# Performance work log

Measured on AMD Instinct MI355X. Metric: run time of the kernel, lower is better.

The kernel has to match this reference:

```python
import jax, jax.numpy as jnp
import numpy as np
from jax import lax

BS, EN, SEQ = 512, 512, 64
D_ENT, D_IN, D_KEY, D_F, H = 256, 1024, 32, 256, 32


def _layer_norm(x, g, b, eps=1e-5):
    m = x.mean(-1, keepdims=True)
    v = ((x - m) ** 2).mean(-1, keepdims=True)
    return (x - m) * lax.rsqrt(v + eps) * g + b


def setup_inputs() -> dict:
    key = jax.random.key(0)
    ks = jax.random.split(key, 24)
    f32 = jnp.float32

    def w(k, shape, fan_in):
        return (jax.random.normal(k, shape, dtype=f32) / np.sqrt(fan_in)).astype(f32)

    inp = {
        'entity_embedding': jax.random.normal(ks[0], (BS, EN, D_ENT), dtype=f32),
        'autoregressive_embedding': jax.random.normal(ks[1], (BS, D_IN), dtype=f32),
        'entity_num': jax.random.randint(ks[2], (BS,), 0, EN),
        'selected_units': jax.random.randint(ks[3], (BS, SEQ), 0, EN),
        'selected_units_num': jax.random.randint(ks[4], (BS,), 0, SEQ),
        # fc_block params (Linear: y = x @ W + b)
        'key_fc_w': w(ks[5], (D_ENT, D_KEY), D_ENT), 'key_fc_b': jnp.zeros((D_KEY,), f32),
        'q1_w': w(ks[6], (D_IN, D_F), D_IN), 'q1_b': jnp.zeros((D_F,), f32),
        'q2_w': w(ks[7], (D_F, D_KEY), D_F), 'q2_b': jnp.zeros((D_KEY,), f32),
        'e1_w': w(ks[8], (D_KEY, D_F), D_KEY), 'e1_b': jnp.zeros((D_F,), f32),
        'e2_w': w(ks[9], (D_F, D_IN), D_F), 'e2_b': jnp.zeros((D_IN,), f32),
        'end_embedding': jax.random.uniform(ks[10], (D_KEY,), dtype=f32,
                                            minval=-1.0 / np.sqrt(D_KEY), maxval=1.0 / np.sqrt(D_KEY)),
        # LayerNorm-LSTM (single layer), gate order: i, f, g, o
        'w_ih': w(ks[11], (D_KEY, 4 * H), D_KEY),
        'w_hh': w(ks[12], (H, 4 * H), H),
        'ln_ig': 1.0 + 0.1 * jax.random.normal(ks[13], (4 * H,), dtype=f32),
        'ln_ib': 0.1 * jax.random.normal(ks[14], (4 * H,), dtype=f32),
        'ln_hg': 1.0 + 0.1 * jax.random.normal(ks[15], (4 * H,), dtype=f32),
        'ln_hb': 0.1 * jax.random.normal(ks[16], (4 * H,), dtype=f32),
        'ln_cg': 1.0 + 0.1 * jax.random.normal(ks[17], (H,), dtype=f32),
        'ln_cb': 0.1 * jax.random.normal(ks[18], (H,), dtype=f32),
    }
    return inp


def _forward(entity_embedding, autoregressive_embedding, entity_num, selected_units,
             selected_units_num, key_fc_w, key_fc_b, q1_w, q1_b, q2_w, q2_b,
             e1_w, e1_b, e2_w, e2_b, end_embedding,
             w_ih, w_hh, ln_ig, ln_ib, ln_hg, ln_hb, ln_cg, ln_cb):
    bs = entity_embedding.shape[0]
    ar = jnp.arange(bs)
    # _get_key_mask: keys for all entities + zero pad slot, end_embedding at slot entity_num
    key = entity_embedding @ key_fc_w + key_fc_b                      # [bs, EN, Dk]
    key = jnp.concatenate([key, jnp.zeros((bs, 1, key.shape[-1]), key.dtype)], axis=1)  # [bs, EN+1, Dk]
    key = key.at[ar, entity_num].set(end_embedding.astype(key.dtype))
    key_embeddings = key                                              # reduce_type == 'selected_units_num'
    base_mask = jnp.arange(key.shape[1])[None, :] < (entity_num + 1)[:, None]  # sequence_mask(entity_num+1)
    mask0 = base_mask.at[ar, entity_num].set(False)                   # end token masked at step 0
    su_prev = jnp.concatenate([selected_units[:, :1], selected_units[:, :-1]], axis=1)

    def step(carry, xs):
        mask, ae, end_flag, one_hot, h, c = carry
        i, su_i, su_p = xs
        # teacher-forced mask evolution
        m1 = jnp.where(i == 1, mask.at[ar, entity_num].set(True), mask)
        m2 = m1.at[ar, su_p].set(False)
        mask = jnp.where(i > 0, m2, mask)
        # query_fc2(query_fc1(ae)) -> LN-LSTM cell
        x = jnp.maximum(ae @ q1_w + q1_b, 0.0) @ q2_w + q2_b
        gates = _layer_norm(x @ w_ih, ln_ig, ln_ib) + _layer_norm(h @ w_hh, ln_hg, ln_hb)
        ig, fg, cg, og = jnp.split(gates, 4, axis=-1)
        c = _layer_norm(jax.nn.sigmoid(fg) * c + jax.nn.sigmoid(ig) * jnp.tanh(cg), ln_cg, ln_cb)
        h = jax.nn.sigmoid(og) * jnp.tanh(c)
        # one-hot scatter of selected unit (skipped once end token seen)
        end_flag = end_flag | (su_i == entity_num)
        one_hot = one_hot.at[ar, su_i].max((~end_flag).astype(one_hot.dtype))
        # mean-pooled embedding of selected units -> embed_fc -> new ae
        emb = jnp.einsum('bn,bnd->bd', one_hot, key_embeddings)
        cnt = one_hot.sum(-1)
        denom = jnp.where((selected_units_num != 0) & (cnt > 0), cnt, 1.0)
        emb = emb / denom[:, None]
        ae = autoregressive_embedding + (jnp.maximum(emb @ e1_w + e1_b, 0.0) @ e2_w + e2_b)
        return (mask, ae, end_flag, one_hot, h, c), (h, mask)

    carry0 = (mask0, autoregressive_embedding,
              jnp.zeros((bs,), bool), jnp.zeros((bs, key.shape[1]), key.dtype),
              jnp.zeros((bs, w_hh.shape[0]), key.dtype), jnp.zeros((bs, w_hh.shape[0]), key.dtype))
    xs = (jnp.arange(selected_units.shape[1]), selected_units.T, su_prev.T)
    _, (queries, masks) = lax.scan(step, carry0, xs)   # [S,bs,Dk], [S,bs,EN+1]
    logits = jnp.einsum('sbd,bnd->sbn', queries, key)
    logits = jnp.where(masks, logits, jnp.asarray(-1e9, logits.dtype))
    return logits.transpose(1, 0, 2)                   # [bs, S, EN+1]


def reference(entity_embedding, autoregressive_embedding, entity_num, selected_units,
              selected_units_num, key_fc_w, key_fc_b, q1_w, q1_b, q2_w, q2_b,
              e1_w, e1_b, e2_w, e2_b, end_embedding,
              w_ih, w_hh, ln_ig, ln_ib, ln_hg, ln_hb, ln_cg, ln_cb):
    return _forward(entity_embedding, autoregressive_embedding, entity_num, selected_units,
                    selected_units_num, key_fc_w, key_fc_b, q1_w, q1_b, q2_w, q2_b,
                    e1_w, e1_b, e2_w, e2_b, end_embedding,
                    w_ih, w_hh, ln_ig, ln_ib, ln_hg, ln_hb, ln_cg, ln_cb)
```

## Files before the change

### kernel.cpp

```cpp
#include <hip/hip_runtime.h>
#include <cstdint>
#include <cstddef>


typedef short bf16x8 __attribute__((ext_vector_type(8)));
typedef float f32x4  __attribute__((ext_vector_type(4)));

__device__ __forceinline__ unsigned f2bf2(float lo, float hi) {
    unsigned r;
    asm("v_cvt_pk_bf16_f32 %0, %1, %2" : "=v"(r) : "v"(lo), "v"(hi));
    return r;
}
__device__ __forceinline__ ushort f2bf(float f) {
    unsigned r;
    asm("v_cvt_pk_bf16_f32 %0, %1, %1" : "=v"(r) : "v"(f));
    return (ushort)r;
}

__device__ __forceinline__ void gld16(const void* g, void* l) {
    __builtin_amdgcn_global_load_lds(
        (const __attribute__((address_space(1))) void*)g,
        (__attribute__((address_space(3))) void*)l,
        16, 0, 0);
}

template<int BM, int BN, int BK, int WR, int WC,
         bool RELU, bool ADDVEC, bool OUT_BF16, bool A_F32, bool KEYMODE>
__global__ __launch_bounds__(WR * WC * 64)
void mfma_gemm(const void* __restrict__ Av, int lda,
               const ushort* __restrict__ BT,
               const float* __restrict__ bias,
               const float* __restrict__ addvec, int ldadd,
               void* __restrict__ outv, int ldo,
               int K, int out_row_offset)
{
    constexpr int NT  = WR * WC * 64;
    constexpr int WM  = BM / WR, WN = BN / WC;
    constexpr int TMt = WM / 16, TNt = WN / 16;
    constexpr int KC  = BK / 8;
    constexpr int CHA = BM * KC, CHB = BN * KC;
    __shared__ __align__(16) ushort As[BM * BK];
    __shared__ __align__(16) ushort Bs[BN * BK];

    const int tid  = threadIdx.x;
    const int lane = tid & 63;
    const int w    = tid >> 6;
    const int wr   = w / WC, wc = w % WC;
    const int row0 = blockIdx.x * BM;
    const int n0   = blockIdx.y * BN;

    f32x4 acc[TMt][TNt];
#pragma unroll
    for (int i = 0; i < TMt; i++)
#pragma unroll
        for (int j = 0; j < TNt; j++)
#pragma unroll
            for (int r = 0; r < 4; r++) acc[i][j][r] = 0.f;

    const ushort* Ab = (const ushort*)Av;
    const float*  Af = (const float*)Av;

    for (int k0 = 0; k0 < K; k0 += BK) {
        if (A_F32) {
#pragma unroll
            for (int id = tid; id < CHA; id += NT) {
                int r = id / KC, kc = id % KC;
                const float* src = Af + (size_t)(row0 + r) * lda + k0 + kc * 8;
                float4 v0 = *(const float4*)(src);
                float4 v1 = *(const float4*)(src + 4);
                uint4 p;
                p.x = f2bf2(v0.x, v0.y);
                p.y = f2bf2(v0.z, v0.w);
                p.z = f2bf2(v1.x, v1.y);
                p.w = f2bf2(v1.z, v1.w);
                *(uint4*)(&As[id * 8]) = p;
            }
        } else {
#pragma unroll
            for (int id = tid; id < CHA; id += NT) {
                int r = id / KC, kc = id % KC;
                gld16(Ab + (size_t)(row0 + r) * lda + k0 + kc * 8, &As[id * 8]);
            }
        }
#pragma unroll
        for (int id = tid; id < CHB; id += NT) {
            int r = id / KC, kc = id % KC;
            gld16(BT + (size_t)(n0 + r) * K + k0 + kc * 8, &Bs[id * 8]);
        }
        __syncthreads();

        bf16x8 afr[TMt], bfr[TNt];
        const int krd = (lane >> 4) * 8;
        const int mrd = lane & 15;
#pragma unroll
        for (int tm = 0; tm < TMt; tm++)
            afr[tm] = *(bf16x8*)(&As[(wr * WM + tm * 16 + mrd) * BK + krd]);
#pragma unroll
        for (int tn = 0; tn < TNt; tn++)
            bfr[tn] = *(bf16x8*)(&Bs[(wc * WN + tn * 16 + mrd) * BK + krd]);
#pragma unroll
        for (int tm = 0; tm < TMt; tm++)
#pragma unroll
            for (int tn = 0; tn < TNt; tn++)
                acc[tm][tn] = __builtin_amdgcn_mfma_f32_16x16x32_bf16(
                    afr[tm], bfr[tn], acc[tm][tn], 0, 0, 0);
        __syncthreads();
    }

    float*  outf = (float*)outv;
    ushort* outh = (ushort*)outv;
    const int cn = lane & 15;
    const int rb = (lane >> 4) * 4;
#pragma unroll
    for (int tm = 0; tm < TMt; tm++) {
#pragma unroll
        for (int r = 0; r < 4; r++) {
            int grow = row0 + wr * WM + tm * 16 + rb + r;
            int b_   = grow & 511;
#pragma unroll
            for (int tn = 0; tn < TNt; tn++) {
                int gcol = n0 + wc * WN + tn * 16 + cn;
                float v = acc[tm][tn][r] + bias[gcol];
                if (RELU)   v = fmaxf(v, 0.f);
                if (ADDVEC) v += addvec[(size_t)b_ * ldadd + gcol];
                size_t oidx;
                if (KEYMODE) oidx = ((size_t)(grow >> 9) * 513 + b_) * 32 + gcol;
                else         oidx = (size_t)(grow + out_row_offset) * ldo + gcol;
                if (OUT_BF16) outh[oidx] = f2bf(v);
                else          outf[oidx] = v;
            }
        }
    }
}

__global__ __launch_bounds__(256) void misc_prep(
    const float* __restrict__ kw,  const float* __restrict__ e1w,
    const float* __restrict__ e2w, const float* __restrict__ q1w,
    const float* __restrict__ q2w,
    ushort* __restrict__ kwt,  ushort* __restrict__ e1wt,
    ushort* __restrict__ e2wt, ushort* __restrict__ q1wt,
    ushort* __restrict__ q2wt,
    const float* __restrict__ ar, ushort* __restrict__ AEb)
{
    int bx = blockIdx.x;
    if (bx < 512) {
        int i = (bx * 256 + threadIdx.x) * 4;
        float4 v = *(const float4*)(ar + i);
        uint2 o;
        o.x = f2bf2(v.x, v.y);
        o.y = f2bf2(v.z, v.w);
        *(uint2*)(AEb + i) = o;
        return;
    }
    bx -= 512;
    const float* W; ushort* WT; int K, N, t0;
    if      (bx < 8)   { W = kw;  WT = kwt;  K = 256;  N = 32;   t0 = bx; }
    else if (bx < 16)  { W = e1w; WT = e1wt; K = 32;   N = 256;  t0 = bx - 8; }
    else if (bx < 272) { W = e2w; WT = e2wt; K = 256;  N = 1024; t0 = bx - 16; }
    else if (bx < 528) { W = q1w; WT = q1wt; K = 1024; N = 256;  t0 = bx - 272; }
    else               { W = q2w; WT = q2wt; K = 256;  N = 32;   t0 = bx - 528; }
    int nn = N >> 5;
    int kt = (t0 / nn) * 32, nt = (t0 % nn) * 32;
    __shared__ float t[32][33];
    int x = threadIdx.x & 31, y = threadIdx.x >> 5;
    for (int i = y; i < 32; i += 8) t[i][x] = W[(size_t)(kt + i) * N + nt + x];
    __syncthreads();
    for (int i = y; i < 32; i += 8) WT[(size_t)(nt + i) * K + kt + x] = f2bf(t[x][i]);
}

__global__ __launch_bounds__(64) void prep_kernel(
    const int* __restrict__ en_g, const int* __restrict__ su_g,
    const int* __restrict__ sun_g, float* __restrict__ key,
    const float* __restrict__ eemb,
    int* __restrict__ fs_g, ushort* __restrict__ EMB)
{
    int b = blockIdx.x;
    int tid = threadIdx.x;
    __shared__ int fs_l[513];
    __shared__ int su_l[64];
    __shared__ float krows[64 * 32];
    for (int i = tid; i < 513; i += 64) fs_l[i] = 64;
    su_l[tid] = su_g[b * 64 + tid];
    int en = en_g[b];
    if (tid < 32) key[((size_t)b * 513 + 512) * 32 + tid] = 0.f;
    else          key[((size_t)b * 513 + en) * 32 + (tid - 32)] = eemb[tid - 32];
    __syncthreads();
    atomicMin(&fs_l[su_l[tid]], tid);
    unsigned long long ball = __ballot(su_l[tid] == en);
    int T = ball ? (__ffsll(ball) - 1) : 64;
    __syncthreads();
    {
        int d = tid & 31;
#pragma unroll 4
        for (int i = 0; i < 32; i++) {
            int r = 2 * i + (tid >> 5);
            krows[r * 32 + d] = key[((size_t)b * 513 + su_l[r]) * 32 + d];
        }
    }
    for (int i = tid; i < 513; i += 64) fs_g[(size_t)b * 513 + i] = fs_l[i];
    __syncthreads();

    int sun = sun_g[b];
    float a = 0.f;
    int cnt = 0;
    for (int i = 0; i < 64; i++) {
        bool nw = (i < T) && (fs_l[su_l[i]] == i);
        if (nw) {
            cnt++;
            if (tid < 32) a += krows[i * 32 + tid];
        }
        float denom = (sun != 0 && cnt > 0) ? (float)cnt : 1.0f;
        if (tid < 32) EMB[((size_t)i * 512 + b) * 32 + tid] = f2bf(a / denom);
    }
}

__device__ inline float sigm(float x) { return 1.0f / (1.0f + expf(-x)); }

__global__ __launch_bounds__(128) void lstm_kernel(
    const float* __restrict__ X, const float* __restrict__ wih_g,
    const float* __restrict__ whh_g,
    const float* __restrict__ lnig, const float* __restrict__ lnib,
    const float* __restrict__ lnhg, const float* __restrict__ lnhb,
    const float* __restrict__ lncg, const float* __restrict__ lncb,
    float* __restrict__ Q)
{
    const int wv = threadIdx.x >> 6;
    const int lane = threadIdx.x & 63;
    const int b = blockIdx.x * 2 + wv;
    __shared__ float xs[2][64 * 32];

    {
        int d = lane & 31;
#pragma unroll 8
        for (int i = 0; i < 32; i++) {
            int s = 2 * i + (lane >> 5);
            xs[wv][s * 32 + d] = X[((size_t)s * 512 + b) * 32 + d];
        }
    }
    float w0[32], w1[32], u0[32], u1[32];
#pragma unroll
    for (int k = 0; k < 32; k++) {
        w0[k] = wih_g[k * 128 + lane];
        w1[k] = wih_g[k * 128 + lane + 64];
        u0[k] = whh_g[k * 128 + lane];
        u1[k] = whh_g[k * 128 + lane + 64];
    }
    const float gi0 = lnig[lane], gi1 = lnig[lane + 64];
    const float bi0 = lnib[lane], bi1 = lnib[lane + 64];
    const float gh0 = lnhg[lane], gh1 = lnhg[lane + 64];
    const float bh0 = lnhb[lane], bh1 = lnhb[lane + 64];
    const int j = lane & 31;
    const float gc = lncg[j], bc = lncb[j];
    float h = 0.f, c = 0.f;
    __syncthreads();

    const float* xrow = &xs[wv][0];
    for (int s = 0; s < 64; s++) {
        float ax0 = 0.f, ax1 = 0.f, ah0 = 0.f, ah1 = 0.f;
#pragma unroll
        for (int k = 0; k < 32; k++) {
            float xk = xrow[s * 32 + k];
            float hk = __shfl(h, k);
            ax0 += xk * w0[k]; ax1 += xk * w1[k];
            ah0 += hk * u0[k]; ah1 += hk * u1[k];
        }
        float r0 = ax0 + ax1, r1 = ax0 * ax0 + ax1 * ax1;
        float r2 = ah0 + ah1, r3 = ah0 * ah0 + ah1 * ah1;
#pragma unroll
        for (int m = 1; m <= 32; m <<= 1) {
            r0 += __shfl_xor(r0, m); r1 += __shfl_xor(r1, m);
            r2 += __shfl_xor(r2, m); r3 += __shfl_xor(r3, m);
        }
        float mx = r0 * (1.f / 128.f), vx = r1 * (1.f / 128.f) - mx * mx;
        float mh = r2 * (1.f / 128.f), vh = r3 * (1.f / 128.f) - mh * mh;
        float sx = rsqrtf(vx + 1e-5f), sh = rsqrtf(vh + 1e-5f);
        float g0 = (ax0 - mx) * sx * gi0 + bi0 + (ah0 - mh) * sh * gh0 + bh0;
        float g1 = (ax1 - mx) * sx * gi1 + bi1 + (ah1 - mh) * sh * gh1 + bh1;
        float igv = __shfl(g0, j),      fgv = __shfl(g0, j + 32);
        float cgv = __shfl(g1, j),      ogv = __shfl(g1, j + 32);
        float cc = sigm(fgv) * c + sigm(igv) * tanhf(cgv);
        float s0 = cc, s1 = cc * cc;
#pragma unroll
        for (int m = 1; m <= 32; m <<= 1) {
            s0 += __shfl_xor(s0, m); s1 += __shfl_xor(s1, m);
        }
        float mc = s0 * (1.f / 64.f), vc = s1 * (1.f / 64.f) - mc * mc;
        c = (cc - mc) * rsqrtf(vc + 1e-5f) * gc + bc;
        h = sigm(ogv) * tanhf(c);
        if (lane < 32) Q[((size_t)b * 64 + s) * 32 + lane] = h;
    }
}

__global__ __launch_bounds__(128) void logits_kernel(
    const float* __restrict__ key, const float* __restrict__ Q,
    const int* __restrict__ fs_g, const int* __restrict__ en_g,
    float* __restrict__ out)
{
    int b = blockIdx.x;
    int n0 = blockIdx.y * 128;
    int tid = threadIdx.x;
    __shared__ float Qs[64 * 32];
    __shared__ float Ks[128 * 33];
    for (int i = tid * 4; i < 2048; i += 512)
        *(float4*)(&Qs[i]) = *(const float4*)(Q + (size_t)b * 2048 + i);
    for (int i = tid; i < 4096; i += 128) {
        int r = i >> 5, d = i & 31;
        int n = n0 + r;
        Ks[r * 33 + d] = (n < 513) ? key[((size_t)b * 513 + n) * 32 + d] : 0.f;
    }
    __syncthreads();
    int n = n0 + tid;
    if (n < 513) {
        int en = en_g[b];
        int f = fs_g[(size_t)b * 513 + n];
        float kreg[32];
#pragma unroll
        for (int d = 0; d < 32; d++) kreg[d] = Ks[tid * 33 + d];
        for (int s = 0; s < 64; s++) {
            float a = 0.f;
#pragma unroll
            for (int d = 0; d < 32; d++) a += Qs[s * 32 + d] * kreg[d];
            bool m = (s == 0) ? (n < en) : ((n <= en) && (f >= s));
            out[((size_t)b * 64 + s) * 513 + n] = m ? a : -1e9f;
        }
    }
}

extern "C" void kernel_launch(void* const* d_in, const int* in_sizes, int n_in,
                              void* d_out, int out_size, void* d_ws, size_t ws_size,
                              hipStream_t stream)
{
    const float* ee   = (const float*)d_in[0];
    const float* ar   = (const float*)d_in[1];
    const int*   en   = (const int*)d_in[2];
    const int*   su   = (const int*)d_in[3];
    const int*   sun  = (const int*)d_in[4];
    const float* kw   = (const float*)d_in[5];
    const float* kb   = (const float*)d_in[6];
    const float* q1w  = (const float*)d_in[7];
    const float* q1b  = (const float*)d_in[8];
    const float* q2w  = (const float*)d_in[9];
    const float* q2b  = (const float*)d_in[10];
    const float* e1w  = (const float*)d_in[11];
    const float* e1b  = (const float*)d_in[12];
    const float* e2w  = (const float*)d_in[13];
    const float* e2b  = (const float*)d_in[14];
    const float* eemb = (const float*)d_in[15];
    const float* wih  = (const float*)d_in[16];
    const float* whh  = (const float*)d_in[17];
    const float* lnig = (const float*)d_in[18];
    const float* lnib = (const float*)d_in[19];
    const float* lnhg = (const float*)d_in[20];
    const float* lnhb = (const float*)d_in[21];
    const float* lncg = (const float*)d_in[22];
    const float* lncb = (const float*)d_in[23];
    float* outp = (float*)d_out;

    char* p = (char*)d_ws;
    float*  key  = (float*)p;  p += (size_t)512 * 513 * 32 * 4;
    ushort* AEb  = (ushort*)p; p += (size_t)32768 * 1024 * 2;
    ushort* Z1b  = (ushort*)p; p += (size_t)32768 * 256 * 2;
    ushort* EMBb = (ushort*)p; p += (size_t)32768 * 32 * 2;
    float*  X    = (float*)p;  p += (size_t)32768 * 32 * 4;
    float*  Q    = (float*)p;  p += (size_t)32768 * 32 * 4;
    int*    fs   = (int*)p;    p += (size_t)512 * 513 * 4;
    ushort* kwt  = (ushort*)p; p += (size_t)32 * 256 * 2;
    ushort* e1wt = (ushort*)p; p += (size_t)256 * 32 * 2;
    ushort* e2wt = (ushort*)p; p += (size_t)1024 * 256 * 2;
    ushort* q1wt = (ushort*)p; p += (size_t)256 * 1024 * 2;
    ushort* q2wt = (ushort*)p; p += (size_t)32 * 256 * 2;

    misc_prep<<<1048, 256, 0, stream>>>(kw, e1w, e2w, q1w, q2w,
                                        kwt, e1wt, e2wt, q1wt, q2wt, ar, AEb);

    mfma_gemm<128, 32, 32, 4, 1, false, false, false, true, true>
        <<<dim3(2048, 1), 256, 0, stream>>>(ee, 256, kwt, kb, nullptr, 0, key, 32, 256, 0);
    prep_kernel<<<512, 64, 0, stream>>>(en, su, sun, key, eemb, fs, EMBb);

    mfma_gemm<128, 128, 32, 2, 2, true, false, true, false, false>
        <<<dim3(252, 2), 256, 0, stream>>>(EMBb, 32, e1wt, e1b, nullptr, 0, Z1b, 256, 32, 0);
    mfma_gemm<128, 128, 32, 2, 2, false, true, true, false, false>
        <<<dim3(252, 8), 256, 0, stream>>>(Z1b, 256, e2wt, e2b, ar, 1024, AEb, 1024, 256, 512);
    mfma_gemm<128, 128, 32, 2, 2, true, false, true, false, false>
        <<<dim3(256, 2), 256, 0, stream>>>(AEb, 1024, q1wt, q1b, nullptr, 0, Z1b, 256, 1024, 0);
    mfma_gemm<128, 32, 32, 4, 1, false, false, false, false, false>
        <<<dim3(256, 1), 256, 0, stream>>>(Z1b, 256, q2wt, q2b, nullptr, 0, X, 32, 256, 0);

    lstm_kernel<<<256, 128, 0, stream>>>(X, wih, whh, lnig, lnib, lnhg, lnhb, lncg, lncb, Q);

    logits_kernel<<<dim3(512, 5), 128, 0, stream>>>(key, Q, fs, en, outp);
}
```

Baseline: 699.0 us.

## Swizzle GEMM LDS tiles, raise BK, add A-panel-resident e2 GEMM kernel

Adds an XOR swizzle to the LDS layout of the generic MFMA GEMM to cut bank conflicts on fragment reads, and generalises the inner loop so BK can be raised to 64 for several GEMMs. It adds a dedicated kernel for the e2 projection that keeps a 64x256 A panel in LDS and loops over all eight N tiles, so A is loaded once instead of once per N block. It also vectorises Q reads from LDS in the logits kernel. The price is more LDS per block, which may lower occupancy, plus a serial N loop inside the new kernel.

```diff
diff --git a/kernel.cpp b/kernel.cpp
--- a/kernel.cpp
+++ b/kernel.cpp
@@ -38,6 +38,7 @@
     constexpr int WM  = BM / WR, WN = BN / WC;
     constexpr int TMt = WM / 16, TNt = WN / 16;
     constexpr int KC  = BK / 8;
+    constexpr int SWZ = KC - 1;
     constexpr int CHA = BM * KC, CHB = BN * KC;
     __shared__ __align__(16) ushort As[BM * BK];
     __shared__ __align__(16) ushort Bs[BN * BK];
@@ -65,7 +66,8 @@
 #pragma unroll
             for (int id = tid; id < CHA; id += NT) {
                 int r = id / KC, kc = id % KC;
-                const float* src = Af + (size_t)(row0 + r) * lda + k0 + kc * 8;
+                int kcs = kc ^ (r & SWZ);
+                const float* src = Af + (size_t)(row0 + r) * lda + k0 + kcs * 8;
                 float4 v0 = *(const float4*)(src);
                 float4 v1 = *(const float4*)(src + 4);
                 uint4 p;
@@ -79,31 +81,42 @@
 #pragma unroll
             for (int id = tid; id < CHA; id += NT) {
                 int r = id / KC, kc = id % KC;
-                gld16(Ab + (size_t)(row0 + r) * lda + k0 + kc * 8, &As[id * 8]);
+                int kcs = kc ^ (r & SWZ);
+                gld16(Ab + (size_t)(row0 + r) * lda + k0 + kcs * 8, &As[id * 8]);
             }
         }
 #pragma unroll
         for (int id = tid; id < CHB; id += NT) {
             int r = id / KC, kc = id % KC;
-            gld16(BT + (size_t)(n0 + r) * K + k0 + kc * 8, &Bs[id * 8]);
+            int kcs = kc ^ (r & SWZ);
+            gld16(BT + (size_t)(n0 + r) * K + k0 + kcs * 8, &Bs[id * 8]);
         }
         __syncthreads();
 
-        bf16x8 afr[TMt], bfr[TNt];
-        const int krd = (lane >> 4) * 8;
-        const int mrd = lane & 15;
-#pragma unroll
-        for (int tm = 0; tm < TMt; tm++)
-            afr[tm] = *(bf16x8*)(&As[(wr * WM + tm * 16 + mrd) * BK + krd]);
-#pragma unroll
-        for (int tn = 0; tn < TNt; tn++)
-            bfr[tn] = *(bf16x8*)(&Bs[(wc * WN + tn * 16 + mrd) * BK + krd]);
-#pragma unroll
-        for (int tm = 0; tm < TMt; tm++)
-#pragma unroll
-            for (int tn = 0; tn < TNt; tn++)
-                acc[tm][tn] = __builtin_amdgcn_mfma_f32_16x16x32_bf16(
-                    afr[tm], bfr[tn], acc[tm][tn], 0, 0, 0);
+        const int m16 = lane & 15;
+        const int hi  = lane >> 4;
+#pragma unroll
+        for (int kk = 0; kk < BK / 32; kk++) {
+            bf16x8 afr[TMt], bfr[TNt];
+#pragma unroll
+            for (int tm = 0; tm < TMt; tm++) {
+                int row = wr * WM + tm * 16 + m16;
+                int cc  = kk * 4 + hi;
+                afr[tm] = *(bf16x8*)(&As[row * BK + ((cc ^ (row & SWZ)) << 3)]);
+            }
+#pragma unroll
+            for (int tn = 0; tn < TNt; tn++) {
+                int row = wc * WN + tn * 16 + m16;
+                int cc  = kk * 4 + hi;
+                bfr[tn] = *(bf16x8*)(&Bs[row * BK + ((cc ^ (row & SWZ)) << 3)]);
+            }
+#pragma unroll
+            for (int tm = 0; tm < TMt; tm++)
+#pragma unroll
+                for (int tn = 0; tn < TNt; tn++)
+                    acc[tm][tn] = __builtin_amdgcn_mfma_f32_16x16x32_bf16(
+                        afr[tm], bfr[tn], acc[tm][tn], 0, 0, 0);
+        }
         __syncthreads();
     }
 
@@ -128,6 +141,94 @@
                 else         oidx = (size_t)(grow + out_row_offset) * ldo + gcol;
                 if (OUT_BF16) outh[oidx] = f2bf(v);
                 else          outf[oidx] = v;
+            }
+        }
+    }
+}
+
+__global__ __launch_bounds__(256) void gemm_g4_panel(
+    const ushort* __restrict__ Z1,
+    const ushort* __restrict__ BT,
+    const float* __restrict__ bias,
+    const float* __restrict__ ar,
+    ushort* __restrict__ out)
+{
+    __shared__ __align__(16) ushort Ap[64 * 256];
+    __shared__ __align__(16) ushort Bs[128 * 64];
+
+    const int tid  = threadIdx.x;
+    const int lane = tid & 63;
+    const int w    = tid >> 6;
+    const int wr   = w >> 1, wc = w & 1;
+    const int row0 = blockIdx.x * 64;
+
+#pragma unroll
+    for (int id = tid; id < 2048; id += 256) {
+        int r = id >> 5, c = id & 31;
+        int cs = c ^ (r & 7);
+        gld16(Z1 + (size_t)(row0 + r) * 256 + cs * 8, &Ap[id * 8]);
+    }
+    __syncthreads();
+
+    const int m16 = lane & 15;
+    const int hi  = lane >> 4;
+    const int cn  = lane & 15;
+    const int rb  = (lane >> 4) * 4;
+
+    for (int by = 0; by < 8; by++) {
+        f32x4 acc[2][4];
+#pragma unroll
+        for (int i = 0; i < 2; i++)
+#pragma unroll
+            for (int j = 0; j < 4; j++)
+#pragma unroll
+                for (int r = 0; r < 4; r++) acc[i][j][r] = 0.f;
+
+        for (int k0 = 0; k0 < 256; k0 += 64) {
+#pragma unroll
+            for (int id = tid; id < 1024; id += 256) {
+                int r = id >> 3, c = id & 7;
+                int cs = c ^ (r & 7);
+                gld16(BT + (size_t)(by * 128 + r) * 256 + k0 + cs * 8, &Bs[id * 8]);
+            }
+            __syncthreads();
+#pragma unroll
+            for (int kk = 0; kk < 2; kk++) {
+                bf16x8 afr[2], bfr[4];
+#pragma unroll
+                for (int tm = 0; tm < 2; tm++) {
+                    int row = wr * 32 + tm * 16 + m16;
+                    int cc  = (k0 >> 3) + kk * 4 + hi;
+                    afr[tm] = *(bf16x8*)(&Ap[row * 256 + ((cc ^ (row & 7)) << 3)]);
+                }
+#pragma unroll
+                for (int tn = 0; tn < 4; tn++) {
+                    int row = wc * 64 + tn * 16 + m16;
+                    int cc  = kk * 4 + hi;
+                    bfr[tn] = *(bf16x8*)(&Bs[row * 64 + ((cc ^ (row & 7)) << 3)]);
+                }
+#pragma unroll
+                for (int tm = 0; tm < 2; tm++)
+#pragma unroll
+                    for (int tn = 0; tn < 4; tn++)
+                        acc[tm][tn] = __builtin_amdgcn_mfma_f32_16x16x32_bf16(
+                            afr[tm], bfr[tn], acc[tm][tn], 0, 0, 0);
+            }
+            __syncthreads();
+        }
+#pragma unroll
+        for (int tm = 0; tm < 2; tm++) {
+#pragma unroll
+            for (int r = 0; r < 4; r++) {
+                int grow = row0 + wr * 32 + tm * 16 + rb + r;
+                int b_   = grow & 511;
+#pragma unroll
+                for (int tn = 0; tn < 4; tn++) {
+                    int gcol = by * 128 + wc * 64 + tn * 16 + cn;
+                    float v = acc[tm][tn][r] + bias[gcol]
+                            + ar[(size_t)b_ * 1024 + gcol];
+                    out[(size_t)(grow + 512) * 1024 + gcol] = f2bf(v);
+                }
             }
         }
     }
@@ -319,7 +420,11 @@
         for (int s = 0; s < 64; s++) {
             float a = 0.f;
 #pragma unroll
-            for (int d = 0; d < 32; d++) a += Qs[s * 32 + d] * kreg[d];
+            for (int d4 = 0; d4 < 8; d4++) {
+                f32x4 qv = *(const f32x4*)(&Qs[s * 32 + d4 * 4]);
+                a += qv[0] * kreg[d4 * 4 + 0] + qv[1] * kreg[d4 * 4 + 1]
+                   + qv[2] * kreg[d4 * 4 + 2] + qv[3] * kreg[d4 * 4 + 3];
+            }
             bool m = (s == 0) ? (n < en) : ((n <= en) && (f >= s));
             out[((size_t)b * 64 + s) * 513 + n] = m ? a : -1e9f;
         }
@@ -373,17 +478,16 @@
     misc_prep<<<1048, 256, 0, stream>>>(kw, e1w, e2w, q1w, q2w,
                                         kwt, e1wt, e2wt, q1wt, q2wt, ar, AEb);
 
-    mfma_gemm<128, 32, 32, 4, 1, false, false, false, true, true>
+    mfma_gemm<128, 32, 64, 4, 1, false, false, false, true, true>
         <<<dim3(2048, 1), 256, 0, stream>>>(ee, 256, kwt, kb, nullptr, 0, key, 32, 256, 0);
     prep_kernel<<<512, 64, 0, stream>>>(en, su, sun, key, eemb, fs, EMBb);
 
     mfma_gemm<128, 128, 32, 2, 2, true, false, true, false, false>
         <<<dim3(252, 2), 256, 0, stream>>>(EMBb, 32, e1wt, e1b, nullptr, 0, Z1b, 256, 32, 0);
-    mfma_gemm<128, 128, 32, 2, 2, false, true, true, false, false>
-        <<<dim3(252, 8), 256, 0, stream>>>(Z1b, 256, e2wt, e2b, ar, 1024, AEb, 1024, 256, 512);
-    mfma_gemm<128, 128, 32, 2, 2, true, false, true, false, false>
+    gemm_g4_panel<<<504, 256, 0, stream>>>(Z1b, e2wt, e2b, ar, AEb);
+    mfma_gemm<128, 128, 64, 2, 2, true, false, true, false, false>
         <<<dim3(256, 2), 256, 0, stream>>>(AEb, 1024, q1wt, q1b, nullptr, 0, Z1b, 256, 1024, 0);
-    mfma_gemm<128, 32, 32, 4, 1, false, false, false, false, false>
+    mfma_gemm<128, 32, 64, 4, 1, false, false, false, false, false>
         <<<dim3(256, 1), 256, 0, stream>>>(Z1b, 256, q2wt, q2b, nullptr, 0, X, 32, 256, 0);
 
     lstm_kernel<<<256, 128, 0, stream>>>(X, wih, whh, lnig, lnib, lnhg, lnhb, lncg, lncb, Q);
```

Result: no change. 695.5 us (-0.5%).
